# Kernel optimization log

Measured on AMD Instinct MI355X. Metric: run time of the kernel, lower is better.

Reference implementation:

```python
import jax, jax.numpy as jnp
import numpy as np

HIDDEN = 2048
INTER = 1408
N_ROUTED = 32
N_SHARED = 2
TOP_K = 6
B, S = 2, 1024


def setup_inputs() -> dict:
    key = jax.random.key(0)
    ks = jax.random.split(key, 9)
    scale = 0.02
    x = jax.random.normal(ks[0], (B, S, HIDDEN), dtype=jnp.float32)
    w_router = jax.random.normal(ks[1], (HIDDEN, N_ROUTED), dtype=jnp.float32) * scale
    wg = jax.random.normal(ks[2], (N_ROUTED, HIDDEN, INTER), dtype=jnp.float32) * scale
    wu = jax.random.normal(ks[3], (N_ROUTED, HIDDEN, INTER), dtype=jnp.float32) * scale
    wd = jax.random.normal(ks[4], (N_ROUTED, INTER, HIDDEN), dtype=jnp.float32) * scale
    sg = jax.random.normal(ks[5], (N_SHARED, HIDDEN, INTER), dtype=jnp.float32) * scale
    su = jax.random.normal(ks[6], (N_SHARED, HIDDEN, INTER), dtype=jnp.float32) * scale
    sd = jax.random.normal(ks[7], (N_SHARED, INTER, HIDDEN), dtype=jnp.float32) * scale
    return {"x": x, "w_router": w_router, "wg": wg, "wu": wu, "wd": wd,
            "sg": sg, "su": su, "sd": sd}


def _swiglu(xf, wg_e, wu_e, wd_e):
    # xf: [T, D]; wg_e/wu_e: [D, F]; wd_e: [F, D]
    h = jax.nn.silu(xf @ wg_e) * (xf @ wu_e)
    return h @ wd_e


def reference(x, w_router, wg, wu, wd, sg, su, sd):
    Bb, Ss, D = x.shape
    xf = x.reshape(-1, D)                      # [T, D], T = B*S
    T = xf.shape[0]

    # Shared experts: applied densely to every token, summed.
    shared = jnp.zeros_like(xf)
    for i in range(sg.shape[0]):               # small fixed count (2)
        shared = shared + _swiglu(xf, sg[i], su[i], sd[i])

    # Router: softmax over all routed experts, then top-k + renormalize.
    probs = jax.nn.softmax(xf @ w_router, axis=-1)            # [T, E]
    topw, topi = jax.lax.top_k(probs, TOP_K)                  # [T, K]
    topw = topw / jnp.sum(topw, axis=-1, keepdims=True)

    # Dense [T, E] combine weights (zero where expert not selected).
    E = wg.shape[0]
    wdense = jnp.zeros((T, E), dtype=xf.dtype)
    wdense = wdense.at[jnp.arange(T)[:, None], topi].add(topw)

    # Scan over experts, accumulating weighted expert outputs (memory-light).
    def body(acc, ew):
        wg_e, wu_e, wd_e, w_e = ew            # w_e: [T] combine weight for this expert
        y = _swiglu(xf, wg_e, wu_e, wd_e)     # [T, D]
        return acc + w_e[:, None] * y, None

    routed, _ = jax.lax.scan(body, jnp.zeros_like(xf), (wg, wu, wd, wdense.T))

    return (shared + routed).reshape(Bb, Ss, D)
```

## Files before the change

### kernel.cpp

```cpp
#include <hip/hip_runtime.h>
#include <hip/hip_bf16.h>

#define T_TOK 2048
#define D_HID 2048
#define F_INT 1408
#define N_EXP 32
#define TOPK 6
#define NJOBS 34
#define SH_BASE 12288
#define ROWS_TOTAL 16384
#define XP_ROWS 14336
#define MAXT_GU 159
#define GU_NBN 22
#define MAXT_DN 159
#define LDSW 40

typedef __bf16 bf16;
typedef __bf16 bf16x4 __attribute__((ext_vector_type(4)));
typedef __bf16 bf16x8 __attribute__((ext_vector_type(8)));
typedef float f32x4 __attribute__((ext_vector_type(4)));

#define WAITBAR() asm volatile("s_waitcnt vmcnt(4) lgkmcnt(0)\n\ts_barrier" ::: "memory")

__device__ __forceinline__ void gll16(const bf16* g, bf16* l) {
    __builtin_amdgcn_global_load_lds((const __attribute__((address_space(1))) void*)g,
                                     (__attribute__((address_space(3))) void*)l, 16, 0, 0);
}

__device__ __forceinline__ int swz16(int r, int k) {
    return r * LDSW + ((((k >> 3) ^ ((r >> 3) & 3) ^ ((r >> 5) & 3)) & 3) << 3) + (k & 7);
}
__device__ __forceinline__ int aslot(int r) { return (r + (r >> 2)) & 3; }

__device__ __forceinline__ int decode_tile(const int* __restrict__ counts, int bid,
                                           int NBN, int MSH, int NSH,
                                           int& job, int& n0, int& m0) {
    int total = 0;
    for (int j = 0; j < NJOBS; ++j) {
        int c = (j < N_EXP) ? counts[j] : T_TOK;
        total += ((c + (1 << MSH) - 1) >> MSH) * NBN;
    }
    if (bid >= total) return 0;
    int q = total >> 3, r = total & 7, x = bid & 7, o = bid >> 3;
    int L = (x < r ? x * (q + 1) : r * (q + 1) + (x - r) * q) + o;
    int acc = 0;
    for (int j = 0; j < NJOBS; ++j) {
        int c = (j < N_EXP) ? counts[j] : T_TOK;
        int tc = (c + (1 << MSH) - 1) >> MSH;
        int b = tc * NBN;
        if (L < acc + b) {
            int rem = L - acc;
            int n0i = rem / tc;
            job = j;
            n0 = n0i << NSH;
            m0 = (rem - n0i * tc) << MSH;
            return 1;
        }
        acc += b;
    }
    return 0;
}

__global__ __launch_bounds__(256) void k_router(const float* __restrict__ x,
                                                const float* __restrict__ wr,
                                                int* __restrict__ counts,
                                                int* __restrict__ tok_e,
                                                float* __restrict__ tok_w) {
    int t = blockIdx.x;
    int tid = threadIdx.x;
    __shared__ float xs[D_HID];
    __shared__ float part[8][32];
    __shared__ float probs[N_EXP];

    const float4* xsrc = (const float4*)(x + (size_t)t * D_HID);
    float4* xdst = (float4*)xs;
    for (int i = tid; i < D_HID / 4; i += 256) xdst[i] = xsrc[i];
    __syncthreads();

    int e = tid & 31, c = tid >> 5;
    float p = 0.f;
    const float* wp = wr + e;
    #pragma unroll 8
    for (int h = c * 256; h < c * 256 + 256; ++h) p += xs[h] * wp[h * 32];
    part[c][e] = p;
    __syncthreads();

    if (tid < 32) {
        float l = 0.f;
        #pragma unroll
        for (int cc = 0; cc < 8; ++cc) l += part[cc][tid];
        float m = l;
        for (int off = 16; off; off >>= 1) m = fmaxf(m, __shfl_xor(m, off));
        float ex = __expf(l - m);
        float s = ex;
        for (int off = 16; off; off >>= 1) s += __shfl_xor(s, off);
        probs[tid] = ex / s;
    }
    __syncthreads();

    if (tid == 0) {
        unsigned used = 0;
        int ids[TOPK]; float wsv[TOPK]; float wsum = 0.f;
        for (int k = 0; k < TOPK; ++k) {
            int best = 0; float bv = -1.f;
            for (int ee = 0; ee < N_EXP; ++ee)
                if (!((used >> ee) & 1u) && probs[ee] > bv) { bv = probs[ee]; best = ee; }
            used |= 1u << best;
            ids[k] = best; wsv[k] = bv; wsum += bv;
        }
        float inv = 1.f / wsum;
        for (int k = 0; k < TOPK; ++k) {
            tok_e[t * TOPK + k] = ids[k];
            tok_w[t * TOPK + k] = wsv[k] * inv;
            atomicAdd(&counts[ids[k]], 1);
        }
    }
}

__global__ void k_plan(const int* __restrict__ counts, int* __restrict__ offs,
                       int* __restrict__ cursors) {
    int tid = threadIdx.x;
    if (tid < N_EXP) cursors[tid] = 0;
    if (tid == 0) {
        int o = 0;
        offs[0] = 0;
        for (int e2 = 0; e2 < N_EXP; ++e2) { o += counts[e2]; offs[e2 + 1] = o; }
        offs[33] = offs[32] + T_TOK;
        offs[34] = offs[33] + T_TOK;
    }
}

__global__ __launch_bounds__(256) void k_assign(const int* __restrict__ tok_e,
                                                const int* __restrict__ offs,
                                                int* __restrict__ cursors,
                                                int* __restrict__ slots,
                                                int* __restrict__ rowtok) {
    int t = blockIdx.x * 256 + threadIdx.x;
    #pragma unroll
    for (int k = 0; k < TOPK; ++k) {
        int e = tok_e[t * TOPK + k];
        int pos = atomicAdd(&cursors[e], 1);
        int slot = offs[e] + pos;
        slots[t * TOPK + k] = slot;
        rowtok[slot] = t;
    }
    rowtok[SH_BASE + t] = t;
    rowtok[SH_BASE + T_TOK + t] = t;
}

__global__ __launch_bounds__(256) void k_gather(const float* __restrict__ x,
                                                const int* __restrict__ rowtok,
                                                bf16* __restrict__ Xp) {
    int s = blockIdx.x;
    int src = (s < SH_BASE) ? rowtok[s] : (s - SH_BASE);
    const float* xr = x + (size_t)src * D_HID + threadIdx.x * 8;
    float4 f0 = *(const float4*)xr;
    float4 f1 = *(const float4*)(xr + 4);
    bf16x8 v = {(bf16)f0.x, (bf16)f0.y, (bf16)f0.z, (bf16)f0.w,
                (bf16)f1.x, (bf16)f1.y, (bf16)f1.z, (bf16)f1.w};
    *(bf16x8*)(Xp + (size_t)s * D_HID + threadIdx.x * 8) = v;
}

__global__ __launch_bounds__(256) void k_xcvt(const float* __restrict__ x,
                                              bf16* __restrict__ xb) {
    int i = blockIdx.x * 2048 + threadIdx.x * 8;
    float4 f0 = *(const float4*)(x + i);
    float4 f1 = *(const float4*)(x + i + 4);
    bf16x8 v = {(bf16)f0.x, (bf16)f0.y, (bf16)f0.z, (bf16)f0.w,
                (bf16)f1.x, (bf16)f1.y, (bf16)f1.z, (bf16)f1.w};
    *(bf16x8*)(xb + i) = v;
}

__global__ __launch_bounds__(256, 4) void k_gateup(
    const bf16* __restrict__ xp, const float* __restrict__ wg, const float* __restrict__ wu,
    const float* __restrict__ sg, const float* __restrict__ su,
    const int* __restrict__ rowtok, const int* __restrict__ counts, const int* __restrict__ offs,
    bf16* __restrict__ H, int dense) {

    int job, n0, m0;
    if (!decode_tile(counts, blockIdx.x, GU_NBN, 7, 6, job, n0, m0)) return;
    int cnt = (job < N_EXP) ? counts[job] : T_TOK;
    int base = offs[job];
    const float* Wg = (job < N_EXP) ? wg + (size_t)job * D_HID * F_INT
                                    : sg + (size_t)(job - N_EXP) * D_HID * F_INT;
    const float* Wu = (job < N_EXP) ? wu + (size_t)job * D_HID * F_INT
                                    : su + (size_t)(job - N_EXP) * D_HID * F_INT;

    __shared__ bf16 As[2][128 * 32];
    __shared__ bf16 Bg[2][64 * LDSW];
    __shared__ bf16 Bu[2][64 * LDSW];

    int tid = threadIdx.x;
    int lane = tid & 63;
    int wid = tid >> 6;
    int wm = (wid & 1) * 64;
    int wn = (wid >> 1) * 32;

    const bf16* agsrc[2];
    #pragma unroll
    for (int i = 0; i < 2; ++i) {
        int rl = wid * 32 + i * 16 + (lane >> 2);
        int grow = m0 + rl; if (grow > cnt - 1) grow = cnt - 1;
        int arow = dense ? (((job < N_EXP) ? base : SH_BASE) + grow)
                         : rowtok[base + grow];
        int kslot = (lane & 3) ^ aslot(rl);
        agsrc[i] = xp + (size_t)arow * D_HID + kslot * 8;
    }

    int sub = tid & 127;
    int nn = (sub & 15) * 4;
    int k4 = (sub >> 4) * 4;
    const float* wsrc = ((tid & 128) ? Wu : Wg) + (size_t)k4 * F_INT + n0 + nn;

    int q = lane >> 4;
    int aoff[4], boff[2];
    #pragma unroll
    for (int mf = 0; mf < 4; ++mf) {
        int R = wm + mf * 16 + (lane & 15);
        aoff[mf] = R * 32 + ((q ^ aslot(R)) << 3);
    }
    #pragma unroll
    for (int nf = 0; nf < 2; ++nf)
        boff[nf] = swz16(wn + nf * 16 + (lane & 15), q * 8);

    f32x4 accg[4][2], accu[4][2];
    f32x4 zero = {0.f, 0.f, 0.f, 0.f};
    #pragma unroll
    for (int i = 0; i < 4; ++i)
        #pragma unroll
        for (int j = 0; j < 2; ++j) { accg[i][j] = zero; accu[i][j] = zero; }

    float4 rb[4];

    auto GLLA = [&](int s, int t) {
        gll16(agsrc[0] + t * 32, &As[s][wid * 1024]);
        gll16(agsrc[1] + t * 32, &As[s][wid * 1024 + 512]);
    };
    auto LOADB = [&](int t) {
        const float* b0 = wsrc + (size_t)(t * 32) * F_INT;
        rb[0] = *(const float4*)b0;
        rb[1] = *(const float4*)(b0 + F_INT);
        rb[2] = *(const float4*)(b0 + 2 * F_INT);
        rb[3] = *(const float4*)(b0 + 3 * F_INT);
    };
    auto WRITEB = [&](int s) {
        bf16* bd = (tid & 128) ? Bu[s] : Bg[s];
        bf16x4 p0 = {(bf16)rb[0].x, (bf16)rb[1].x, (bf16)rb[2].x, (bf16)rb[3].x};
        bf16x4 p1 = {(bf16)rb[0].y, (bf16)rb[1].y, (bf16)rb[2].y, (bf16)rb[3].y};
        bf16x4 p2 = {(bf16)rb[0].z, (bf16)rb[1].z, (bf16)rb[2].z, (bf16)rb[3].z};
        bf16x4 p3 = {(bf16)rb[0].w, (bf16)rb[1].w, (bf16)rb[2].w, (bf16)rb[3].w};
        *(bf16x4*)&bd[swz16(nn + 0, k4)] = p0;
        *(bf16x4*)&bd[swz16(nn + 1, k4)] = p1;
        *(bf16x4*)&bd[swz16(nn + 2, k4)] = p2;
        *(bf16x4*)&bd[swz16(nn + 3, k4)] = p3;
    };
    auto MM = [&](int cur) {
        bf16x8 af[4];
        #pragma unroll
        for (int mf = 0; mf < 4; ++mf)
            af[mf] = *(const bf16x8*)&As[cur][aoff[mf]];
        #pragma unroll
        for (int nf = 0; nf < 2; ++nf) {
            bf16x8 bfr = *(const bf16x8*)&Bg[cur][boff[nf]];
            bf16x8 ufr = *(const bf16x8*)&Bu[cur][boff[nf]];
            #pragma unroll
            for (int mf = 0; mf < 4; ++mf) {
                accg[mf][nf] = __builtin_amdgcn_mfma_f32_16x16x32_bf16(af[mf], bfr, accg[mf][nf], 0, 0, 0);
                accu[mf][nf] = __builtin_amdgcn_mfma_f32_16x16x32_bf16(af[mf], ufr, accu[mf][nf], 0, 0, 0);
            }
        }
    };

    const int NT = D_HID / 32;
    GLLA(0, 0);
    __builtin_amdgcn_sched_barrier(0);
    LOADB(0);
    WRITEB(0);
    LOADB(1);
    WAITBAR();

    for (int kt = 0; kt < NT; ++kt) {
        int cur = kt & 1, nxt = cur ^ 1;
        int t1 = kt + 1 < NT ? kt + 1 : NT - 1;
        int t2 = kt + 2 < NT ? kt + 2 : NT - 1;
        GLLA(nxt, t1);
        __builtin_amdgcn_sched_barrier(0);
        WRITEB(nxt);
        LOADB(t2);
        MM(cur);
        WAITBAR();
    }

    #pragma unroll
    for (int mf = 0; mf < 4; ++mf) {
        #pragma unroll
        for (int nf = 0; nf < 2; ++nf) {
            int col = n0 + wn + nf * 16 + (lane & 15);
            #pragma unroll
            for (int r = 0; r < 4; ++r) {
                int grow = m0 + wm + mf * 16 + (lane >> 4) * 4 + r;
                if (grow < cnt) {
                    float g = accg[mf][nf][r];
                    float u = accu[mf][nf][r];
                    float h = g * u / (1.f + __expf(-g));
                    H[(size_t)(base + grow) * F_INT + col] = (bf16)h;
                }
            }
        }
    }
}

__global__ __launch_bounds__(256, 4) void k_down(
    const bf16* __restrict__ H, const float* __restrict__ wd, const float* __restrict__ sd,
    const int* __restrict__ counts, const int* __restrict__ offs,
    bf16* __restrict__ P) {

    int job, n0, m0;
    if (!decode_tile(counts, blockIdx.x, D_HID / 128, 7, 7, job, n0, m0)) return;
    int cnt = (job < N_EXP) ? counts[job] : T_TOK;
    int base = offs[job];
    const float* Wd = (job < N_EXP) ? wd + (size_t)job * F_INT * D_HID
                                    : sd + (size_t)(job - N_EXP) * F_INT * D_HID;

    __shared__ bf16 As[2][128 * 32];
    __shared__ bf16 Bs[2][128 * LDSW];

    int tid = threadIdx.x;
    int lane = tid & 63;
    int wid = tid >> 6;
    int wm = (wid >> 1) * 64;
    int wn = (wid & 1) * 64;

    const bf16* agsrc[2];
    #pragma unroll
    for (int i = 0; i < 2; ++i) {
        int rl = wid * 32 + i * 16 + (lane >> 2);
        int grow = m0 + rl; if (grow > cnt - 1) grow = cnt - 1;
        int kslot = (lane & 3) ^ aslot(rl);
        agsrc[i] = H + (size_t)(base + grow) * F_INT + kslot * 8;
    }

    int k4 = (tid >> 5) * 4;
    int nn = (tid & 31) * 4;
    const float* bsrc = Wd + (size_t)k4 * D_HID + n0 + nn;

    int q = lane >> 4;
    int aoff[4], boff[4];
    #pragma unroll
    for (int mf = 0; mf < 4; ++mf) {
        int R = wm + mf * 16 + (lane & 15);
        aoff[mf] = R * 32 + ((q ^ aslot(R)) << 3);
    }
    #pragma unroll
    for (int nf = 0; nf < 4; ++nf)
        boff[nf] = swz16(wn + nf * 16 + (lane & 15), q * 8);

    f32x4 acc[4][4];
    f32x4 zero = {0.f, 0.f, 0.f, 0.f};
    #pragma unroll
    for (int i = 0; i < 4; ++i)
        #pragma unroll
        for (int j = 0; j < 4; ++j) acc[i][j] = zero;

    float4 rb[4];

    auto GLLA = [&](int s, int t) {
        gll16(agsrc[0] + t * 32, &As[s][wid * 1024]);
        gll16(agsrc[1] + t * 32, &As[s][wid * 1024 + 512]);
    };
    auto LOADB = [&](int t) {
        const float* b0 = bsrc + (size_t)(t * 32) * D_HID;
        rb[0] = *(const float4*)b0;
        rb[1] = *(const float4*)(b0 + D_HID);
        rb[2] = *(const float4*)(b0 + 2 * D_HID);
        rb[3] = *(const float4*)(b0 + 3 * D_HID);
    };
    auto WRITEB = [&](int s) {
        bf16x4 p0 = {(bf16)rb[0].x, (bf16)rb[1].x, (bf16)rb[2].x, (bf16)rb[3].x};
        bf16x4 p1 = {(bf16)rb[0].y, (bf16)rb[1].y, (bf16)rb[2].y, (bf16)rb[3].y};
        bf16x4 p2 = {(bf16)rb[0].z, (bf16)rb[1].z, (bf16)rb[2].z, (bf16)rb[3].z};
        bf16x4 p3 = {(bf16)rb[0].w, (bf16)rb[1].w, (bf16)rb[2].w, (bf16)rb[3].w};
        *(bf16x4*)&Bs[s][swz16(nn + 0, k4)] = p0;
        *(bf16x4*)&Bs[s][swz16(nn + 1, k4)] = p1;
        *(bf16x4*)&Bs[s][swz16(nn + 2, k4)] = p2;
        *(bf16x4*)&Bs[s][swz16(nn + 3, k4)] = p3;
    };
    auto MM = [&](int cur) {
        bf16x8 af[4];
        #pragma unroll
        for (int mf = 0; mf < 4; ++mf)
            af[mf] = *(const bf16x8*)&As[cur][aoff[mf]];
        #pragma unroll
        for (int nf = 0; nf < 4; ++nf) {
            bf16x8 bfr = *(const bf16x8*)&Bs[cur][boff[nf]];
            #pragma unroll
            for (int mf = 0; mf < 4; ++mf)
                acc[mf][nf] = __builtin_amdgcn_mfma_f32_16x16x32_bf16(af[mf], bfr, acc[mf][nf], 0, 0, 0);
        }
    };

    const int NT = F_INT / 32;
    GLLA(0, 0);
    __builtin_amdgcn_sched_barrier(0);
    LOADB(0);
    WRITEB(0);
    LOADB(1);
    WAITBAR();

    for (int kt = 0; kt < NT; ++kt) {
        int cur = kt & 1, nxt = cur ^ 1;
        int t1 = kt + 1 < NT ? kt + 1 : NT - 1;
        int t2 = kt + 2 < NT ? kt + 2 : NT - 1;
        GLLA(nxt, t1);
        __builtin_amdgcn_sched_barrier(0);
        WRITEB(nxt);
        LOADB(t2);
        MM(cur);
        WAITBAR();
    }

    #pragma unroll
    for (int mf = 0; mf < 4; ++mf) {
        #pragma unroll
        for (int nf = 0; nf < 4; ++nf) {
            int col = n0 + wn + nf * 16 + (lane & 15);
            #pragma unroll
            for (int r = 0; r < 4; ++r) {
                int grow = m0 + wm + mf * 16 + (lane >> 4) * 4 + r;
                if (grow < cnt)
                    P[(size_t)(base + grow) * D_HID + col] = (bf16)acc[mf][nf][r];
            }
        }
    }
}

__global__ __launch_bounds__(256) void k_combine(const bf16* __restrict__ P,
                                                 const int* __restrict__ slots,
                                                 const float* __restrict__ tok_w,
                                                 float* __restrict__ out) {
    int t = blockIdx.x;
    int tid = threadIdx.x;
    __shared__ int ss[TOPK];
    __shared__ float ww[TOPK];
    if (tid < TOPK) { ss[tid] = slots[t * TOPK + tid]; ww[tid] = tok_w[t * TOPK + tid]; }
    __syncthreads();
    int c0 = tid * 8;
    float acc[8];
    {
        bf16x8 v0 = *(const bf16x8*)(P + (size_t)(SH_BASE + t) * D_HID + c0);
        bf16x8 v1 = *(const bf16x8*)(P + (size_t)(SH_BASE + T_TOK + t) * D_HID + c0);
        #pragma unroll
        for (int i = 0; i < 8; ++i) acc[i] = (float)v0[i] + (float)v1[i];
    }
    #pragma unroll
    for (int k = 0; k < TOPK; ++k) {
        bf16x8 v = *(const bf16x8*)(P + (size_t)ss[k] * D_HID + c0);
        float w = ww[k];
        #pragma unroll
        for (int i = 0; i < 8; ++i) acc[i] += w * (float)v[i];
    }
    float4 o0 = {acc[0], acc[1], acc[2], acc[3]};
    float4 o1 = {acc[4], acc[5], acc[6], acc[7]};
    *(float4*)(out + (size_t)t * D_HID + c0) = o0;
    *(float4*)(out + (size_t)t * D_HID + c0 + 4) = o1;
}

extern "C" void kernel_launch(void* const* d_in, const int* in_sizes, int n_in,
                              void* d_out, int out_size, void* d_ws, size_t ws_size,
                              hipStream_t stream) {
    const float* x  = (const float*)d_in[0];
    const float* wr = (const float*)d_in[1];
    const float* wg = (const float*)d_in[2];
    const float* wu = (const float*)d_in[3];
    const float* wd = (const float*)d_in[4];
    const float* sg = (const float*)d_in[5];
    const float* su = (const float*)d_in[6];
    const float* sd = (const float*)d_in[7];
    float* out = (float*)d_out;

    const size_t H_BYTES  = (size_t)ROWS_TOTAL * F_INT * 2;
    const size_t P_BYTES  = (size_t)ROWS_TOTAL * D_HID * 2;
    const size_t XP_BYTES = (size_t)XP_ROWS * D_HID * 2;

    char* w = (char*)d_ws;
    int*   counts   = (int*)(w + 0);
    int*   cursors  = (int*)(w + 256);
    int*   offs     = (int*)(w + 512);
    int*   tok_e    = (int*)(w + 8192);
    float* tok_w    = (float*)(w + 8192 + 49152);
    int*   slots    = (int*)(w + 8192 + 2 * 49152);
    int*   rowtok   = (int*)(w + 8192 + 3 * 49152);
    bf16*  H        = (bf16*)(w + 262144);
    bf16*  P        = (bf16*)(w + 262144 + H_BYTES);
    bf16*  Xp       = (bf16*)(w + 262144 + H_BYTES + P_BYTES);

    int dense = (ws_size >= 262144 + H_BYTES + P_BYTES + XP_BYTES) ? 1 : 0;

    hipMemsetAsync(counts, 0, 128, stream);
    k_router<<<T_TOK, 256, 0, stream>>>(x, wr, counts, tok_e, tok_w);
    k_plan<<<1, 64, 0, stream>>>(counts, offs, cursors);
    k_assign<<<T_TOK / 256, 256, 0, stream>>>(tok_e, offs, cursors, slots, rowtok);
    if (dense) {
        k_gather<<<XP_ROWS, 256, 0, stream>>>(x, rowtok, Xp);
    } else {
        k_xcvt<<<T_TOK * D_HID / 2048, 256, 0, stream>>>(x, Xp);
    }
    k_gateup<<<MAXT_GU * GU_NBN, 256, 0, stream>>>(
        Xp, wg, wu, sg, su, rowtok, counts, offs, H, dense);
    k_down<<<MAXT_DN * (D_HID / 128), 256, 0, stream>>>(
        H, wd, sd, counts, offs, P);
    k_combine<<<T_TOK, 256, 0, stream>>>(P, slots, tok_w, out);
}
```

Before: 743.7 us.

## Load A fragments directly from global into registers, dropping LDS staging

Both GEMM kernels (gate/up and down) stop staging the activation tile in LDS via global_load_lds and instead load each wave's MFMA A fragments straight from global memory into registers every k-step. This removes the As shared buffers, the swizzle, and the vmcnt wait in the barrier, and occupancy hints drop from 4 to 3 blocks per CU. The cost is that waves sharing rows now reload the same A data from global/L2 without reuse. The A loads are also no longer prefetched a step ahead, so each MFMA step waits on global latency.

```diff
diff --git a/kernel.cpp b/kernel.cpp
--- a/kernel.cpp
+++ b/kernel.cpp
@@ -20,17 +20,11 @@
 typedef __bf16 bf16x8 __attribute__((ext_vector_type(8)));
 typedef float f32x4 __attribute__((ext_vector_type(4)));
 
-#define WAITBAR() asm volatile("s_waitcnt vmcnt(4) lgkmcnt(0)\n\ts_barrier" ::: "memory")
-
-__device__ __forceinline__ void gll16(const bf16* g, bf16* l) {
-    __builtin_amdgcn_global_load_lds((const __attribute__((address_space(1))) void*)g,
-                                     (__attribute__((address_space(3))) void*)l, 16, 0, 0);
-}
+#define BAR() asm volatile("s_waitcnt lgkmcnt(0)\n\ts_barrier" ::: "memory")
 
 __device__ __forceinline__ int swz16(int r, int k) {
     return r * LDSW + ((((k >> 3) ^ ((r >> 3) & 3) ^ ((r >> 5) & 3)) & 3) << 3) + (k & 7);
 }
-__device__ __forceinline__ int aslot(int r) { return (r + (r >> 2)) & 3; }
 
 __device__ __forceinline__ int decode_tile(const int* __restrict__ counts, int bid,
                                            int NBN, int MSH, int NSH,
@@ -171,7 +165,7 @@
     *(bf16x8*)(xb + i) = v;
 }
 
-__global__ __launch_bounds__(256, 4) void k_gateup(
+__global__ __launch_bounds__(256, 3) void k_gateup(
     const bf16* __restrict__ xp, const float* __restrict__ wg, const float* __restrict__ wu,
     const float* __restrict__ sg, const float* __restrict__ su,
     const int* __restrict__ rowtok, const int* __restrict__ counts, const int* __restrict__ offs,
@@ -186,7 +180,6 @@
     const float* Wu = (job < N_EXP) ? wu + (size_t)job * D_HID * F_INT
                                     : su + (size_t)(job - N_EXP) * D_HID * F_INT;
 
-    __shared__ bf16 As[2][128 * 32];
     __shared__ bf16 Bg[2][64 * LDSW];
     __shared__ bf16 Bu[2][64 * LDSW];
 
@@ -195,16 +188,16 @@
     int wid = tid >> 6;
     int wm = (wid & 1) * 64;
     int wn = (wid >> 1) * 32;
-
-    const bf16* agsrc[2];
-    #pragma unroll
-    for (int i = 0; i < 2; ++i) {
-        int rl = wid * 32 + i * 16 + (lane >> 2);
-        int grow = m0 + rl; if (grow > cnt - 1) grow = cnt - 1;
+    int q = lane >> 4;
+
+    const bf16* aptr[4];
+    #pragma unroll
+    for (int mf = 0; mf < 4; ++mf) {
+        int R = wm + mf * 16 + (lane & 15);
+        int grow = m0 + R; if (grow > cnt - 1) grow = cnt - 1;
         int arow = dense ? (((job < N_EXP) ? base : SH_BASE) + grow)
                          : rowtok[base + grow];
-        int kslot = (lane & 3) ^ aslot(rl);
-        agsrc[i] = xp + (size_t)arow * D_HID + kslot * 8;
+        aptr[mf] = xp + (size_t)arow * D_HID + q * 8;
     }
 
     int sub = tid & 127;
@@ -212,13 +205,7 @@
     int k4 = (sub >> 4) * 4;
     const float* wsrc = ((tid & 128) ? Wu : Wg) + (size_t)k4 * F_INT + n0 + nn;
 
-    int q = lane >> 4;
-    int aoff[4], boff[2];
-    #pragma unroll
-    for (int mf = 0; mf < 4; ++mf) {
-        int R = wm + mf * 16 + (lane & 15);
-        aoff[mf] = R * 32 + ((q ^ aslot(R)) << 3);
-    }
+    int boff[2];
     #pragma unroll
     for (int nf = 0; nf < 2; ++nf)
         boff[nf] = swz16(wn + nf * 16 + (lane & 15), q * 8);
@@ -230,11 +217,13 @@
         #pragma unroll
         for (int j = 0; j < 2; ++j) { accg[i][j] = zero; accu[i][j] = zero; }
 
+    bf16x8 af[4];
     float4 rb[4];
 
-    auto GLLA = [&](int s, int t) {
-        gll16(agsrc[0] + t * 32, &As[s][wid * 1024]);
-        gll16(agsrc[1] + t * 32, &As[s][wid * 1024 + 512]);
+    auto LOADAF = [&](int kt) {
+        #pragma unroll
+        for (int mf = 0; mf < 4; ++mf)
+            af[mf] = *(const bf16x8*)(aptr[mf] + kt * 32);
     };
     auto LOADB = [&](int t) {
         const float* b0 = wsrc + (size_t)(t * 32) * F_INT;
@@ -255,10 +244,6 @@
         *(bf16x4*)&bd[swz16(nn + 3, k4)] = p3;
     };
     auto MM = [&](int cur) {
-        bf16x8 af[4];
-        #pragma unroll
-        for (int mf = 0; mf < 4; ++mf)
-            af[mf] = *(const bf16x8*)&As[cur][aoff[mf]];
         #pragma unroll
         for (int nf = 0; nf < 2; ++nf) {
             bf16x8 bfr = *(const bf16x8*)&Bg[cur][boff[nf]];
@@ -272,23 +257,18 @@
     };
 
     const int NT = D_HID / 32;
-    GLLA(0, 0);
-    __builtin_amdgcn_sched_barrier(0);
     LOADB(0);
     WRITEB(0);
     LOADB(1);
-    WAITBAR();
+    BAR();
 
     for (int kt = 0; kt < NT; ++kt) {
         int cur = kt & 1, nxt = cur ^ 1;
-        int t1 = kt + 1 < NT ? kt + 1 : NT - 1;
-        int t2 = kt + 2 < NT ? kt + 2 : NT - 1;
-        GLLA(nxt, t1);
-        __builtin_amdgcn_sched_barrier(0);
-        WRITEB(nxt);
-        LOADB(t2);
+        LOADAF(kt);
+        if (kt + 1 < NT) WRITEB(nxt);
+        if (kt + 2 < NT) LOADB(kt + 2);
         MM(cur);
-        WAITBAR();
+        BAR();
     }
 
     #pragma unroll
@@ -310,7 +290,7 @@
     }
 }
 
-__global__ __launch_bounds__(256, 4) void k_down(
+__global__ __launch_bounds__(256, 3) void k_down(
     const bf16* __restrict__ H, const float* __restrict__ wd, const float* __restrict__ sd,
     const int* __restrict__ counts, const int* __restrict__ offs,
     bf16* __restrict__ P) {
@@ -322,7 +302,6 @@
     const float* Wd = (job < N_EXP) ? wd + (size_t)job * F_INT * D_HID
                                     : sd + (size_t)(job - N_EXP) * F_INT * D_HID;
 
-    __shared__ bf16 As[2][128 * 32];
     __shared__ bf16 Bs[2][128 * LDSW];
 
     int tid = threadIdx.x;
@@ -330,27 +309,21 @@
     int wid = tid >> 6;
     int wm = (wid >> 1) * 64;
     int wn = (wid & 1) * 64;
-
-    const bf16* agsrc[2];
-    #pragma unroll
-    for (int i = 0; i < 2; ++i) {
-        int rl = wid * 32 + i * 16 + (lane >> 2);
-        int grow = m0 + rl; if (grow > cnt - 1) grow = cnt - 1;
-        int kslot = (lane & 3) ^ aslot(rl);
-        agsrc[i] = H + (size_t)(base + grow) * F_INT + kslot * 8;
+    int q = lane >> 4;
+
+    const bf16* aptr[4];
+    #pragma unroll
+    for (int mf = 0; mf < 4; ++mf) {
+        int R = wm + mf * 16 + (lane & 15);
+        int grow = m0 + R; if (grow > cnt - 1) grow = cnt - 1;
+        aptr[mf] = H + (size_t)(base + grow) * F_INT + q * 8;
     }
 
     int k4 = (tid >> 5) * 4;
     int nn = (tid & 31) * 4;
     const float* bsrc = Wd + (size_t)k4 * D_HID + n0 + nn;
 
-    int q = lane >> 4;
-    int aoff[4], boff[4];
-    #pragma unroll
-    for (int mf = 0; mf < 4; ++mf) {
-        int R = wm + mf * 16 + (lane & 15);
-        aoff[mf] = R * 32 + ((q ^ aslot(R)) << 3);
-    }
+    int boff[4];
     #pragma unroll
     for (int nf = 0; nf < 4; ++nf)
         boff[nf] = swz16(wn + nf * 16 + (lane & 15), q * 8);
@@ -362,11 +335,13 @@
         #pragma unroll
         for (int j = 0; j < 4; ++j) acc[i][j] = zero;
 
+    bf16x8 af[4];
     float4 rb[4];
 
-    auto GLLA = [&](int s, int t) {
-        gll16(agsrc[0] + t * 32, &As[s][wid * 1024]);
-        gll16(agsrc[1] + t * 32, &As[s][wid * 1024 + 512]);
+    auto LOADAF = [&](int kt) {
+        #pragma unroll
+        for (int mf = 0; mf < 4; ++mf)
+            af[mf] = *(const bf16x8*)(aptr[mf] + kt * 32);
     };
     auto LOADB = [&](int t) {
         const float* b0 = bsrc + (size_t)(t * 32) * D_HID;
@@ -386,10 +361,6 @@
         *(bf16x4*)&Bs[s][swz16(nn + 3, k4)] = p3;
     };
     auto MM = [&](int cur) {
-        bf16x8 af[4];
-        #pragma unroll
-        for (int mf = 0; mf < 4; ++mf)
-            af[mf] = *(const bf16x8*)&As[cur][aoff[mf]];
         #pragma unroll
         for (int nf = 0; nf < 4; ++nf) {
             bf16x8 bfr = *(const bf16x8*)&Bs[cur][boff[nf]];
@@ -400,23 +371,18 @@
     };
 
     const int NT = F_INT / 32;
-    GLLA(0, 0);
-    __builtin_amdgcn_sched_barrier(0);
     LOADB(0);
     WRITEB(0);
     LOADB(1);
-    WAITBAR();
+    BAR();
 
     for (int kt = 0; kt < NT; ++kt) {
         int cur = kt & 1, nxt = cur ^ 1;
-        int t1 = kt + 1 < NT ? kt + 1 : NT - 1;
-        int t2 = kt + 2 < NT ? kt + 2 : NT - 1;
-        GLLA(nxt, t1);
-        __builtin_amdgcn_sched_barrier(0);
-        WRITEB(nxt);
-        LOADB(t2);
+        LOADAF(kt);
+        if (kt + 1 < NT) WRITEB(nxt);
+        if (kt + 2 < NT) LOADB(kt + 2);
         MM(cur);
-        WAITBAR();
+        BAR();
     }
 
     #pragma unroll
```

Measured after the change: 1.044 ms. 40.3% more time.

## Triple-buffer A tiles and prefetch A fragments in gate/up GEMM

Applied to the files above, without the earlier changes.

The gate/up kernel moves the activation tile to a three-stage LDS ring and issues global-to-LDS loads two K-steps ahead. The A fragments for the next step are read into registers before the current step's MFMAs run. The main loop is unrolled by two with alternating register sets, and the occupancy hint drops from 4 to 3 blocks per CU to make room for the extra registers and LDS. The goal is to hide LDS read latency and the activation load latency behind MFMA work. The cost is lower occupancy and more delicate vmcnt accounting, since the wait still assumes vmcnt(4) while one more load group is in flight.

```diff
diff --git a/kernel.cpp b/kernel.cpp
--- a/kernel.cpp
+++ b/kernel.cpp
@@ -171,7 +171,7 @@
     *(bf16x8*)(xb + i) = v;
 }
 
-__global__ __launch_bounds__(256, 4) void k_gateup(
+__global__ __launch_bounds__(256, 3) void k_gateup(
     const bf16* __restrict__ xp, const float* __restrict__ wg, const float* __restrict__ wu,
     const float* __restrict__ sg, const float* __restrict__ su,
     const int* __restrict__ rowtok, const int* __restrict__ counts, const int* __restrict__ offs,
@@ -186,7 +186,7 @@
     const float* Wu = (job < N_EXP) ? wu + (size_t)job * D_HID * F_INT
                                     : su + (size_t)(job - N_EXP) * D_HID * F_INT;
 
-    __shared__ bf16 As[2][128 * 32];
+    __shared__ bf16 As[3][128 * 32];
     __shared__ bf16 Bg[2][64 * LDSW];
     __shared__ bf16 Bu[2][64 * LDSW];
 
@@ -230,11 +230,12 @@
         #pragma unroll
         for (int j = 0; j < 2; ++j) { accg[i][j] = zero; accu[i][j] = zero; }
 
+    bf16x8 afA[4], afB[4];
     float4 rb[4];
 
-    auto GLLA = [&](int s, int t) {
-        gll16(agsrc[0] + t * 32, &As[s][wid * 1024]);
-        gll16(agsrc[1] + t * 32, &As[s][wid * 1024 + 512]);
+    auto GLLA = [&](int b, int t) {
+        gll16(agsrc[0] + t * 32, &As[b][wid * 1024]);
+        gll16(agsrc[1] + t * 32, &As[b][wid * 1024 + 512]);
     };
     auto LOADB = [&](int t) {
         const float* b0 = wsrc + (size_t)(t * 32) * F_INT;
@@ -254,11 +255,13 @@
         *(bf16x4*)&bd[swz16(nn + 2, k4)] = p2;
         *(bf16x4*)&bd[swz16(nn + 3, k4)] = p3;
     };
-    auto MM = [&](int cur) {
-        bf16x8 af[4];
+    auto PREF = [&](bf16x8 (&dst)[4], int b) {
+        const bf16* ab = &As[b][0];
         #pragma unroll
         for (int mf = 0; mf < 4; ++mf)
-            af[mf] = *(const bf16x8*)&As[cur][aoff[mf]];
+            dst[mf] = *(const bf16x8*)&ab[aoff[mf]];
+    };
+    auto MM = [&](const bf16x8 (&af)[4], int cur) {
         #pragma unroll
         for (int nf = 0; nf < 2; ++nf) {
             bf16x8 bfr = *(const bf16x8*)&Bg[cur][boff[nf]];
@@ -273,22 +276,35 @@
 
     const int NT = D_HID / 32;
     GLLA(0, 0);
+    GLLA(1, 1);
     __builtin_amdgcn_sched_barrier(0);
     LOADB(0);
     WRITEB(0);
     LOADB(1);
-    WAITBAR();
-
-    for (int kt = 0; kt < NT; ++kt) {
-        int cur = kt & 1, nxt = cur ^ 1;
-        int t1 = kt + 1 < NT ? kt + 1 : NT - 1;
-        int t2 = kt + 2 < NT ? kt + 2 : NT - 1;
-        GLLA(nxt, t1);
-        __builtin_amdgcn_sched_barrier(0);
-        WRITEB(nxt);
-        LOADB(t2);
-        MM(cur);
-        WAITBAR();
+    asm volatile("s_waitcnt lgkmcnt(0)\n\ts_barrier" ::: "memory");
+    PREF(afA, 0);
+
+    for (int kt = 0; kt < NT; kt += 2) {
+        {
+            int tg = kt + 2 < NT ? kt + 2 : NT - 1;
+            GLLA((kt + 2) % 3, tg);
+            __builtin_amdgcn_sched_barrier(0);
+            WRITEB(1);
+            LOADB(tg);
+            PREF(afB, (kt + 1) % 3);
+            MM(afA, 0);
+            WAITBAR();
+        }
+        {
+            int tg = kt + 3 < NT ? kt + 3 : NT - 1;
+            GLLA((kt + 3) % 3, tg);
+            __builtin_amdgcn_sched_barrier(0);
+            WRITEB(0);
+            LOADB(tg);
+            PREF(afA, (kt + 2) % 3);
+            MM(afB, 1);
+            WAITBAR();
+        }
     }
 
     #pragma unroll
@@ -405,7 +421,7 @@
     LOADB(0);
     WRITEB(0);
     LOADB(1);
-    WAITBAR();
+    asm volatile("s_waitcnt vmcnt(4) lgkmcnt(0)\n\ts_barrier" ::: "memory");
 
     for (int kt = 0; kt < NT; ++kt) {
         int cur = kt & 1, nxt = cur ^ 1;
@@ -416,7 +432,7 @@
         WRITEB(nxt);
         LOADB(t2);
         MM(cur);
-        WAITBAR();
+        asm volatile("s_waitcnt vmcnt(4) lgkmcnt(0)\n\ts_barrier" ::: "memory");
     }
 
     #pragma unroll
```

Result: no change. 758.0 us (+1.9%).
